# Optimization experiments

Measured on AMD Instinct MI355X. Metric: run time of the kernel, lower is better.

Reference implementation:

```python
import jax, jax.numpy as jnp
import numpy as np

DIM = 1024
N_HEADS = 16
B, S = 2, 2048


def setup_inputs() -> dict:
    key = jax.random.key(0)
    ks = jax.random.split(key, 9)
    scale = 1.0 / np.sqrt(DIM)
    return {
        "i1": jax.random.normal(ks[0], (B, S, DIM), jnp.float32),
        "i2": jax.random.normal(ks[1], (B, S, DIM), jnp.float32),
        "cr": jax.random.normal(ks[2], (B, S, 2), jnp.float32),
        # Linear params stored as [in, out] so forward is x @ W + b (same math as torch x W^T + b)
        "Wq": jax.random.normal(ks[3], (DIM, DIM), jnp.float32) * scale,
        "bq": jnp.zeros((DIM,), jnp.float32),
        "Wkv": jax.random.normal(ks[4], (DIM, 2 * DIM), jnp.float32) * scale,
        "bkv": jnp.zeros((2 * DIM,), jnp.float32),
        "Wmo": jax.random.normal(ks[5], (2, DIM), jnp.float32) * (1.0 / np.sqrt(2.0)),
        "bmo": jnp.zeros((DIM,), jnp.float32),
    }


def reference(i1, i2, cr, Wq, bq, Wkv, bkv, Wmo, bmo):
    H = N_HEADS
    Dh = DIM // H
    b, s, _ = i1.shape

    q = (i1 @ Wq + bq).reshape(b, s, H, Dh)                # [B,S,H,Dh]
    kv = i2 @ Wkv + bkv                                     # [B,S,2*DIM]
    k = kv[..., :DIM].reshape(b, s, H, Dh)
    v = kv[..., DIM:].reshape(b, s, H, Dh)
    mo = (cr @ Wmo + bmo).reshape(b, s, H, Dh)              # [B,S,H,Dh]

    scores = jnp.einsum("bqhd,bkhd->bhqk", q, k) / jnp.sqrt(jnp.asarray(Dh, q.dtype))
    probs = jax.nn.softmax(scores, axis=-1)                 # [B,H,S,S] (dropout p=0)

    h = jnp.einsum("bhqk,bkhd->bqhd", probs, v).reshape(b, s, DIM)
    m = jnp.einsum("bhqk,bkhd->bqhd", probs, mo).reshape(b, s, DIM)
    return h, m
```

## Files before the change

### kernel.cpp

```cpp
#include <hip/hip_runtime.h>
#include <hip/hip_bf16.h>

typedef __attribute__((ext_vector_type(8))) short short8;
typedef __attribute__((ext_vector_type(4))) short short4_t;
typedef __attribute__((ext_vector_type(4))) float f32x4;
typedef unsigned short ushort_t;

#define DEV __device__ __forceinline__

DEV ushort_t f2bf(float f) {
    unsigned u = __builtin_bit_cast(unsigned, f);
    u = u + 0x7fffu + ((u >> 16) & 1u);
    return (ushort_t)(u >> 16);
}

DEV unsigned pk_bf16(float lo, float hi) {
    __hip_bfloat162 h = __float22bfloat162_rn(make_float2(lo, hi));
    unsigned u;
    __builtin_memcpy(&u, &h, sizeof(u));
    return u;
}

DEV float fast_exp2(float x) {
#if __has_builtin(__builtin_amdgcn_exp2f)
    return __builtin_amdgcn_exp2f(x);
#else
    float r;
    asm("v_exp_f32 %0, %1" : "=v"(r) : "v"(x));
    return r;
#endif
}

DEV short8 ld8(const ushort_t* p) { return *reinterpret_cast<const short8*>(p); }

__global__ __launch_bounds__(256)
void cvt_bf16(const float* __restrict__ in, ushort_t* __restrict__ out)
{
    const size_t i = ((size_t)blockIdx.x * 256 + threadIdx.x) * 8;
    const float4 a = *reinterpret_cast<const float4*>(in + i);
    const float4 b = *reinterpret_cast<const float4*>(in + i + 4);
    short8 v;
    v[0] = (short)f2bf(a.x); v[1] = (short)f2bf(a.y);
    v[2] = (short)f2bf(a.z); v[3] = (short)f2bf(a.w);
    v[4] = (short)f2bf(b.x); v[5] = (short)f2bf(b.y);
    v[6] = (short)f2bf(b.z); v[7] = (short)f2bf(b.w);
    *reinterpret_cast<short8*>(out + i) = v;
}

__global__ __launch_bounds__(256)
void tcvt_bf16(const float* __restrict__ W, ushort_t* __restrict__ Wt, int K, int N)
{
    __shared__ ushort_t tile[64][72];
    const int t = threadIdx.x;
    const int nx = blockIdx.x * 64, ky = blockIdx.y * 64;
    const int r = t >> 2, q = (t & 3) * 16;

    const float* src = W + (size_t)(ky + r) * N + nx + q;
#pragma unroll
    for (int i = 0; i < 4; ++i) {
        const float4 v = *reinterpret_cast<const float4*>(src + 4 * i);
        tile[r][q + 4 * i + 0] = f2bf(v.x);
        tile[r][q + 4 * i + 1] = f2bf(v.y);
        tile[r][q + 4 * i + 2] = f2bf(v.z);
        tile[r][q + 4 * i + 3] = f2bf(v.w);
    }
    __syncthreads();
    short8 o0, o1;
#pragma unroll
    for (int i = 0; i < 8; ++i) {
        o0[i] = (short)tile[q + i][r];
        o1[i] = (short)tile[q + 8 + i][r];
    }
    ushort_t* dst = Wt + (size_t)(nx + r) * K + ky + q;
    *reinterpret_cast<short8*>(dst) = o0;
    *reinterpret_cast<short8*>(dst + 8) = o1;
}

__global__ __launch_bounds__(256, 2)
void proj_all(const ushort_t* __restrict__ A1, const ushort_t* __restrict__ A2,
              const ushort_t* __restrict__ Wqt, const ushort_t* __restrict__ Wkvt,
              const float* __restrict__ bqv, const float* __restrict__ bkv,
              ushort_t* __restrict__ Qr, ushort_t* __restrict__ Kr,
              ushort_t* __restrict__ Vt)
{
    __shared__ ushort_t As[128 * 72];
    __shared__ ushort_t Bs[128 * 72];

    const int t = threadIdx.x;
    const int lane = t & 63;
    const int wv = t >> 6;
    const int wr = wv >> 1, wc = wv & 1;
    const int c = lane & 15, g = lane >> 4;
    const int m0 = blockIdx.y * 128;
    const int nblk = blockIdx.x;

    const ushort_t* A;
    const ushort_t* Wt;
    const float* bias;
    int n0;
    if (nblk < 8) { A = A1; Wt = Wqt;  bias = bqv; n0 = nblk * 128; }
    else          { A = A2; Wt = Wkvt; bias = bkv; n0 = (nblk - 8) * 128; }
    const bool isQ = (nblk < 8);

    f32x4 acc[4][4];
    const f32x4 zero4 = {0.f, 0.f, 0.f, 0.f};
#pragma unroll
    for (int mi = 0; mi < 4; ++mi)
#pragma unroll
        for (int ni = 0; ni < 4; ++ni) acc[mi][ni] = zero4;

    const int srow[4] = { (t + 0)   >> 3, (t + 256) >> 3, (t + 512) >> 3, (t + 768) >> 3 };
    const int skq     = (t & 7) * 8;

    short8 a_reg[4], b_reg[4];
#pragma unroll
    for (int rep = 0; rep < 4; ++rep) {
        a_reg[rep] = ld8(A  + (size_t)(m0 + srow[rep]) * 1024 + skq);
        b_reg[rep] = ld8(Wt + (size_t)(n0 + srow[rep]) * 1024 + skq);
    }

    for (int it = 0; it < 16; ++it) {
#pragma unroll
        for (int rep = 0; rep < 4; ++rep) {
            *reinterpret_cast<short8*>(&As[srow[rep] * 72 + skq]) = a_reg[rep];
            *reinterpret_cast<short8*>(&Bs[srow[rep] * 72 + skq]) = b_reg[rep];
        }
        __syncthreads();
        if (it < 15) {
            const int k1 = (it + 1) * 64;
#pragma unroll
            for (int rep = 0; rep < 4; ++rep) {
                a_reg[rep] = ld8(A  + (size_t)(m0 + srow[rep]) * 1024 + k1 + skq);
                b_reg[rep] = ld8(Wt + (size_t)(n0 + srow[rep]) * 1024 + k1 + skq);
            }
        }
#pragma unroll
        for (int kk = 0; kk < 64; kk += 32) {
            short8 afr[4], bfr[4];
#pragma unroll
            for (int mi = 0; mi < 4; ++mi)
                afr[mi] = ld8(&As[(wr * 64 + mi * 16 + c) * 72 + kk + 8 * g]);
#pragma unroll
            for (int ni = 0; ni < 4; ++ni)
                bfr[ni] = ld8(&Bs[(wc * 64 + ni * 16 + c) * 72 + kk + 8 * g]);
#pragma unroll
            for (int mi = 0; mi < 4; ++mi)
#pragma unroll
                for (int ni = 0; ni < 4; ++ni)
                    acc[mi][ni] = __builtin_amdgcn_mfma_f32_16x16x32_bf16(
                        afr[mi], bfr[ni], acc[mi][ni], 0, 0, 0);
        }
        __syncthreads();
    }

#pragma unroll
    for (int mi = 0; mi < 4; ++mi) {
#pragma unroll
        for (int ni = 0; ni < 4; ++ni) {
            const int n = n0 + wc * 64 + ni * 16 + c;
            const float bb = bias[n];
#pragma unroll
            for (int j = 0; j < 4; ++j) {
                const int m = m0 + wr * 64 + mi * 16 + 4 * g + j;
                const int b = m >> 11, s = m & 2047;
                const ushort_t val = f2bf(acc[mi][ni][j] + bb);
                if (isQ) {
                    Qr[((size_t)((b * 16 + (n >> 6)) * 2048 + s)) * 64 + (n & 63)] = val;
                } else if (n < 1024) {
                    Kr[((size_t)((b * 16 + (n >> 6)) * 2048 + s)) * 64 + (n & 63)] = val;
                } else {
                    const int np = n - 1024;
                    Vt[(size_t)((b * 16 + (np >> 6)) * 64 + (np & 63)) * 2048 + s] = val;
                }
            }
        }
    }
}

__global__ __launch_bounds__(256)
void proj_gemm(const float* __restrict__ A, const float* __restrict__ W,
               const float* __restrict__ bias, int N,
               ushort_t* __restrict__ outRow, ushort_t* __restrict__ outT)
{
    __shared__ ushort_t As[128 * 72];
    __shared__ ushort_t Bt[128 * 72];

    const int t = threadIdx.x;
    const int lane = t & 63;
    const int wv = t >> 6;
    const int wr = wv >> 1, wc = wv & 1;
    const int c = lane & 15, g = lane >> 4;
    const int m0 = blockIdx.y * 128, n0 = blockIdx.x * 128;

    f32x4 acc[4][4];
    const f32x4 zero4 = {0.f, 0.f, 0.f, 0.f};
#pragma unroll
    for (int mi = 0; mi < 4; ++mi)
#pragma unroll
        for (int ni = 0; ni < 4; ++ni) acc[mi][ni] = zero4;

    for (int it = 0; it < 16; ++it) {
        const int k0 = it * 64;
        {
            const int kq = (t & 15) * 4;
            int r = t >> 4;
#pragma unroll
            for (int rep = 0; rep < 8; ++rep, r += 16) {
                float4 v = *reinterpret_cast<const float4*>(
                    A + (size_t)(m0 + r) * 1024 + k0 + kq);
                ushort_t* dst = &As[r * 72 + kq];
                dst[0] = f2bf(v.x); dst[1] = f2bf(v.y);
                dst[2] = f2bf(v.z); dst[3] = f2bf(v.w);
            }
        }
        {
            const int nq = (t & 31) * 4;
            const int kr = t >> 5;
#pragma unroll
            for (int rep = 0; rep < 8; ++rep) {
                const int k = kr + 8 * rep;
                float4 v = *reinterpret_cast<const float4*>(
                    W + (size_t)(k0 + k) * N + n0 + nq);
                Bt[(nq + 0) * 72 + k] = f2bf(v.x);
                Bt[(nq + 1) * 72 + k] = f2bf(v.y);
                Bt[(nq + 2) * 72 + k] = f2bf(v.z);
                Bt[(nq + 3) * 72 + k] = f2bf(v.w);
            }
        }
        __syncthreads();
#pragma unroll
        for (int kk = 0; kk < 64; kk += 32) {
            short8 afr[4], bfr[4];
#pragma unroll
            for (int mi = 0; mi < 4; ++mi)
                afr[mi] = ld8(&As[(wr * 64 + mi * 16 + c) * 72 + kk + 8 * g]);
#pragma unroll
            for (int ni = 0; ni < 4; ++ni)
                bfr[ni] = ld8(&Bt[(wc * 64 + ni * 16 + c) * 72 + kk + 8 * g]);
#pragma unroll
            for (int mi = 0; mi < 4; ++mi)
#pragma unroll
                for (int ni = 0; ni < 4; ++ni)
                    acc[mi][ni] = __builtin_amdgcn_mfma_f32_16x16x32_bf16(
                        afr[mi], bfr[ni], acc[mi][ni], 0, 0, 0);
        }
        __syncthreads();
    }

#pragma unroll
    for (int mi = 0; mi < 4; ++mi) {
#pragma unroll
        for (int ni = 0; ni < 4; ++ni) {
            const int n = n0 + wc * 64 + ni * 16 + c;
            const float bb = bias[n];
#pragma unroll
            for (int j = 0; j < 4; ++j) {
                const int m = m0 + wr * 64 + mi * 16 + 4 * g + j;
                const int b = m >> 11, s = m & 2047;
                const ushort_t val = f2bf(acc[mi][ni][j] + bb);
                if (outT != nullptr && n >= 1024) {
                    const int np = n - 1024;
                    const int hh = np >> 6, d = np & 63;
                    outT[(size_t)((b * 16 + hh) * 64 + d) * 2048 + s] = val;
                } else {
                    const int hh = n >> 6, d = n & 63;
                    outRow[((size_t)((b * 16 + hh) * 2048 + s)) * 64 + d] = val;
                }
            }
        }
    }
}

DEV void attn_body(const ushort_t* __restrict__ Kh, const ushort_t* __restrict__ Vh,
                   const float* __restrict__ crb, int kv_next,
                   const ushort_t* KsC, const ushort_t* VsC,
                   ushort_t* KsN, ushort_t* VsN,
                   int c, int g, int rk, int ck, int rv, int cv,
                   const short8 (&bq)[2][2],
                   float4 (&CC)[2][2], float4 (&CN)[2][2],
                   f32x4 (&accv)[2][4], float (&lst)[2],
                   float (&a0s)[2], float (&a1s)[2])
{
    const f32x4 zero4 = {0.f, 0.f, 0.f, 0.f};
    const float SCL = 0.18033688011112042f;

    const short8 kreg = ld8(Kh + (size_t)(kv_next + rk) * 64 + ck);
    const short8 vreg = ld8(Vh + (size_t)rv * 2048 + kv_next + cv);
    {
        const float* cp0 = crb + (size_t)(kv_next + 4 * g) * 2;
        CN[0][0] = *reinterpret_cast<const float4*>(cp0);
        CN[0][1] = *reinterpret_cast<const float4*>(cp0 + 4);
        const float* cp1 = crb + (size_t)(kv_next + 16 + 4 * g) * 2;
        CN[1][0] = *reinterpret_cast<const float4*>(cp1);
        CN[1][1] = *reinterpret_cast<const float4*>(cp1 + 4);
    }
    __builtin_amdgcn_sched_barrier(0);

    short8 KC[2][2];
#pragma unroll
    for (int ct = 0; ct < 2; ++ct)
#pragma unroll
        for (int st = 0; st < 2; ++st)
            KC[ct][st] = ld8(&KsC[(ct * 16 + c) * 72 + st * 32 + 8 * g]);
    short8 VC[4];
#pragma unroll
    for (int dt = 0; dt < 4; ++dt) {
        const short4_t vlo = *reinterpret_cast<const short4_t*>(&VsC[(dt * 16 + c) * 40 + 4 * g]);
        const short4_t vhi = *reinterpret_cast<const short4_t*>(&VsC[(dt * 16 + c) * 40 + 4 * g + 16]);
        VC[dt] = __builtin_shufflevector(vlo, vhi, 0, 1, 2, 3, 4, 5, 6, 7);
    }

    f32x4 sc[2][2];
#pragma unroll
    for (int qt = 0; qt < 2; ++qt)
#pragma unroll
        for (int ct = 0; ct < 2; ++ct) {
            f32x4 z = zero4;
            z = __builtin_amdgcn_mfma_f32_16x16x32_bf16(KC[ct][0], bq[qt][0], z, 0, 0, 0);
            z = __builtin_amdgcn_mfma_f32_16x16x32_bf16(KC[ct][1], bq[qt][1], z, 0, 0, 0);
            sc[qt][ct] = z;
        }

    short8 pa[2];
#pragma unroll
    for (int qt = 0; qt < 2; ++qt) {
        float e[2][4];
        float lc = lst[qt], a0c = a0s[qt], a1c = a1s[qt];
#pragma unroll
        for (int ct = 0; ct < 2; ++ct) {
            const float cr0[4] = {CC[ct][0].x, CC[ct][0].z, CC[ct][1].x, CC[ct][1].z};
            const float cr1[4] = {CC[ct][0].y, CC[ct][0].w, CC[ct][1].y, CC[ct][1].w};
#pragma unroll
            for (int j = 0; j < 4; ++j) {
                const float ev = fast_exp2(sc[qt][ct][j] * SCL);
                e[ct][j] = ev;
                lc  += ev;
                a0c += ev * cr0[j];
                a1c += ev * cr1[j];
            }
        }
        lst[qt] = lc; a0s[qt] = a0c; a1s[qt] = a1c;
        int4 w;
        w.x = (int)pk_bf16(e[0][0], e[0][1]);
        w.y = (int)pk_bf16(e[0][2], e[0][3]);
        w.z = (int)pk_bf16(e[1][0], e[1][1]);
        w.w = (int)pk_bf16(e[1][2], e[1][3]);
        pa[qt] = __builtin_bit_cast(short8, w);
    }

#pragma unroll
    for (int dt = 0; dt < 4; ++dt) {
        accv[0][dt] = __builtin_amdgcn_mfma_f32_16x16x32_bf16(VC[dt], pa[0], accv[0][dt], 0, 0, 0);
        accv[1][dt] = __builtin_amdgcn_mfma_f32_16x16x32_bf16(VC[dt], pa[1], accv[1][dt], 0, 0, 0);
    }

    *reinterpret_cast<short8*>(&KsN[rk * 72 + ck]) = kreg;
    *reinterpret_cast<short8*>(&VsN[rv * 40 + cv]) = vreg;
    __syncthreads();
}

__global__ __launch_bounds__(256, 2)
void attn_kernel(const ushort_t* __restrict__ Qr, const ushort_t* __restrict__ Kr,
                 const ushort_t* __restrict__ Vt, const float* __restrict__ cr,
                 const float* __restrict__ Wmo, const float* __restrict__ bmo,
                 float* __restrict__ out)
{
    __shared__ ushort_t Ks[2][32 * 72];
    __shared__ ushort_t Vs[2][64 * 40];

    const int t = threadIdx.x;
    const int w = t >> 6, lane = t & 63;
    const int c = lane & 15, g = lane >> 4;
    const int rk = t >> 3, ck = (t & 7) * 8;
    const int rv = t >> 2, cv = (t & 3) * 8;

    const int gid = blockIdx.x;
    const int bh = (gid & 7) + 8 * ((gid >> 3) & 3);
    const int xt = gid >> 5;
    const int b = bh >> 4, hh = bh & 15;
    const int qb = xt * 128 + w * 32;

    const ushort_t* Qh = Qr + (size_t)bh * (2048 * 64);
    const ushort_t* Kh = Kr + (size_t)bh * (2048 * 64);
    const ushort_t* Vh = Vt + (size_t)bh * (64 * 2048);
    const float*   crb = cr + (size_t)b * (2048 * 2);

    short8 bq[2][2];
#pragma unroll
    for (int qt = 0; qt < 2; ++qt)
#pragma unroll
        for (int st = 0; st < 2; ++st)
            bq[qt][st] = ld8(Qh + (size_t)(qb + qt * 16 + c) * 64 + st * 32 + 8 * g);

    f32x4 accv[2][4];
    const f32x4 zero4 = {0.f, 0.f, 0.f, 0.f};
#pragma unroll
    for (int qt = 0; qt < 2; ++qt)
#pragma unroll
        for (int dt = 0; dt < 4; ++dt) accv[qt][dt] = zero4;

    float lst[2] = {0.f, 0.f};
    float a0s[2] = {0.f, 0.f};
    float a1s[2] = {0.f, 0.f};

    float4 cA[2][2], cB[2][2];

    {
        const short8 k0 = ld8(Kh + (size_t)rk * 64 + ck);
        const short8 v0 = ld8(Vh + (size_t)rv * 2048 + cv);
        *reinterpret_cast<short8*>(&Ks[0][rk * 72 + ck]) = k0;
        *reinterpret_cast<short8*>(&Vs[0][rv * 40 + cv]) = v0;
        const float* cp0 = crb + (size_t)(4 * g) * 2;
        cA[0][0] = *reinterpret_cast<const float4*>(cp0);
        cA[0][1] = *reinterpret_cast<const float4*>(cp0 + 4);
        const float* cp1 = crb + (size_t)(16 + 4 * g) * 2;
        cA[1][0] = *reinterpret_cast<const float4*>(cp1);
        cA[1][1] = *reinterpret_cast<const float4*>(cp1 + 4);
    }
    __syncthreads();

    for (int i = 0; i < 32; ++i) {
        const int kvb = i * 64;
        attn_body(Kh, Vh, crb, kvb + 32,
                  &Ks[0][0], &Vs[0][0], &Ks[1][0], &Vs[1][0],
                  c, g, rk, ck, rv, cv, bq, cA, cB,
                  accv, lst, a0s, a1s);
        attn_body(Kh, Vh, crb, (kvb + 64) & 2047,
                  &Ks[1][0], &Vs[1][0], &Ks[0][0], &Vs[0][0],
                  c, g, rk, ck, rv, cv, bq, cB, cA,
                  accv, lst, a0s, a1s);
    }

#pragma unroll
    for (int qt = 0; qt < 2; ++qt) {
        lst[qt] += __shfl_xor(lst[qt], 16, 64); lst[qt] += __shfl_xor(lst[qt], 32, 64);
        a0s[qt] += __shfl_xor(a0s[qt], 16, 64); a0s[qt] += __shfl_xor(a0s[qt], 32, 64);
        a1s[qt] += __shfl_xor(a1s[qt], 16, 64); a1s[qt] += __shfl_xor(a1s[qt], 32, 64);
    }

#pragma unroll
    for (int qt = 0; qt < 2; ++qt) {
        const int q = qb + qt * 16 + c;
        const float inv = 1.f / lst[qt];
        const float a0 = a0s[qt] * inv, a1 = a1s[qt] * inv;
#pragma unroll
        for (int dt = 0; dt < 4; ++dt) {
            const int d = hh * 64 + dt * 16 + 4 * g;
            const float4 w0 = *reinterpret_cast<const float4*>(Wmo + d);
            const float4 w1 = *reinterpret_cast<const float4*>(Wmo + 1024 + d);
            const float4 bm = *reinterpret_cast<const float4*>(bmo + d);
            const size_t oidx = ((size_t)(b * 2048 + q)) * 1024 + d;
            float4 hv, mv;
            hv.x = accv[qt][dt][0] * inv; hv.y = accv[qt][dt][1] * inv;
            hv.z = accv[qt][dt][2] * inv; hv.w = accv[qt][dt][3] * inv;
            mv.x = a0 * w0.x + a1 * w1.x + bm.x;
            mv.y = a0 * w0.y + a1 * w1.y + bm.y;
            mv.z = a0 * w0.z + a1 * w1.z + bm.z;
            mv.w = a0 * w0.w + a1 * w1.w + bm.w;
            *reinterpret_cast<float4*>(out + oidx) = hv;
            *reinterpret_cast<float4*>(out + 4194304 + oidx) = mv;
        }
    }
}

extern "C" void kernel_launch(void* const* d_in, const int* in_sizes, int n_in,
                              void* d_out, int out_size, void* d_ws, size_t ws_size,
                              hipStream_t stream)
{
    const float* i1  = (const float*)d_in[0];
    const float* i2  = (const float*)d_in[1];
    const float* cr  = (const float*)d_in[2];
    const float* Wq  = (const float*)d_in[3];
    const float* bq  = (const float*)d_in[4];
    const float* Wkv = (const float*)d_in[5];
    const float* bkv = (const float*)d_in[6];
    const float* Wmo = (const float*)d_in[7];
    const float* bmo = (const float*)d_in[8];
    float* out = (float*)d_out;

    ushort_t* Qr = (ushort_t*)d_ws;
    ushort_t* Kr = Qr + 4194304;
    ushort_t* Vt = Kr + 4194304;

    if (ws_size >= 48234496ULL) {
        ushort_t* A1   = Vt + 4194304;
        ushort_t* A2   = A1 + 4194304;
        ushort_t* Wqt  = A2 + 4194304;
        ushort_t* Wkvt = Wqt + 1048576;
        cvt_bf16<<<dim3(2048), dim3(256), 0, stream>>>(i1, A1);
        cvt_bf16<<<dim3(2048), dim3(256), 0, stream>>>(i2, A2);
        tcvt_bf16<<<dim3(16, 16), dim3(256), 0, stream>>>(Wq, Wqt, 1024, 1024);
        tcvt_bf16<<<dim3(32, 16), dim3(256), 0, stream>>>(Wkv, Wkvt, 1024, 2048);
        proj_all<<<dim3(24, 32), dim3(256), 0, stream>>>(A1, A2, Wqt, Wkvt, bq, bkv, Qr, Kr, Vt);
    } else {
        proj_gemm<<<dim3(8, 32), dim3(256), 0, stream>>>(i1, Wq, bq, 1024, Qr, nullptr);
        proj_gemm<<<dim3(16, 32), dim3(256), 0, stream>>>(i2, Wkv, bkv, 2048, Kr, Vt);
    }
    attn_kernel<<<dim3(512), dim3(256), 0, stream>>>(Qr, Kr, Vt, cr, Wmo, bmo, out);
}
```

Before: 132.4 us.

## Split attention KV range across warp pairs and double grid size

Each block now handles 64 queries instead of 128, and its four warps split into two query groups times two KV halves. Each warp pair streams half of the 2048 keys into its own double-buffered shared tiles. Partial accumulators, row sums and cr-weighted sums are then merged through shared memory before the epilogue. The grid doubles to 1024 blocks and launch bounds ask for 4 blocks per CU, raising parallelism and occupancy. In exchange, each K/V tile is loaded by twice as many blocks, there is an extra reduction step, and the tighter occupancy target adds register pressure.

```diff
diff --git a/kernel.cpp b/kernel.cpp
--- a/kernel.cpp
+++ b/kernel.cpp
@@ -271,11 +271,13 @@
     }
 }
 
-DEV void attn_body(const ushort_t* __restrict__ Kh, const ushort_t* __restrict__ Vh,
-                   const float* __restrict__ crb, int kv_next,
+DEV void attn_body(const ushort_t* __restrict__ khh, const ushort_t* __restrict__ vhh,
+                   const float* __restrict__ crh, int kv_next,
                    const ushort_t* KsC, const ushort_t* VsC,
                    ushort_t* KsN, ushort_t* VsN,
-                   int c, int g, int rk, int ck, int rv, int cv,
+                   int c, int g,
+                   int krow0, int krow1, int kcol,
+                   int vrow0, int vrow1, int vcol,
                    const short8 (&bq)[2][2],
                    float4 (&CC)[2][2], float4 (&CN)[2][2],
                    f32x4 (&accv)[2][4], float (&lst)[2],
@@ -284,13 +286,15 @@
     const f32x4 zero4 = {0.f, 0.f, 0.f, 0.f};
     const float SCL = 0.18033688011112042f;
 
-    const short8 kreg = ld8(Kh + (size_t)(kv_next + rk) * 64 + ck);
-    const short8 vreg = ld8(Vh + (size_t)rv * 2048 + kv_next + cv);
+    const short8 kreg0 = ld8(khh + (size_t)(kv_next + krow0) * 64 + kcol);
+    const short8 kreg1 = ld8(khh + (size_t)(kv_next + krow1) * 64 + kcol);
+    const short8 vreg0 = ld8(vhh + (size_t)vrow0 * 2048 + kv_next + vcol);
+    const short8 vreg1 = ld8(vhh + (size_t)vrow1 * 2048 + kv_next + vcol);
     {
-        const float* cp0 = crb + (size_t)(kv_next + 4 * g) * 2;
+        const float* cp0 = crh + (size_t)(kv_next + 4 * g) * 2;
         CN[0][0] = *reinterpret_cast<const float4*>(cp0);
         CN[0][1] = *reinterpret_cast<const float4*>(cp0 + 4);
-        const float* cp1 = crb + (size_t)(kv_next + 16 + 4 * g) * 2;
+        const float* cp1 = crh + (size_t)(kv_next + 16 + 4 * g) * 2;
         CN[1][0] = *reinterpret_cast<const float4*>(cp1);
         CN[1][1] = *reinterpret_cast<const float4*>(cp1 + 4);
     }
@@ -354,37 +358,51 @@
         accv[1][dt] = __builtin_amdgcn_mfma_f32_16x16x32_bf16(VC[dt], pa[1], accv[1][dt], 0, 0, 0);
     }
 
-    *reinterpret_cast<short8*>(&KsN[rk * 72 + ck]) = kreg;
-    *reinterpret_cast<short8*>(&VsN[rv * 40 + cv]) = vreg;
+    *reinterpret_cast<short8*>(&KsN[krow0 * 72 + kcol]) = kreg0;
+    *reinterpret_cast<short8*>(&KsN[krow1 * 72 + kcol]) = kreg1;
+    *reinterpret_cast<short8*>(&VsN[vrow0 * 40 + vcol]) = vreg0;
+    *reinterpret_cast<short8*>(&VsN[vrow1 * 40 + vcol]) = vreg1;
     __syncthreads();
 }
 
-__global__ __launch_bounds__(256, 2)
+__global__ __launch_bounds__(256, 4)
 void attn_kernel(const ushort_t* __restrict__ Qr, const ushort_t* __restrict__ Kr,
                  const ushort_t* __restrict__ Vt, const float* __restrict__ cr,
                  const float* __restrict__ Wmo, const float* __restrict__ bmo,
                  float* __restrict__ out)
 {
-    __shared__ ushort_t Ks[2][32 * 72];
-    __shared__ ushort_t Vs[2][64 * 40];
+    __shared__ short8 smem16[2432];
+    ushort_t* smem = (ushort_t*)smem16;
 
     const int t = threadIdx.x;
     const int w = t >> 6, lane = t & 63;
+    const int wq = w & 1, wk = w >> 1;
     const int c = lane & 15, g = lane >> 4;
-    const int rk = t >> 3, ck = (t & 7) * 8;
-    const int rv = t >> 2, cv = (t & 3) * 8;
+    const int th = t & 127;
+
+    const int krow0 = th >> 3,          krow1 = (th + 128) >> 3, kcol = (th & 7) * 8;
+    const int vrow0 = th >> 2,          vrow1 = (th + 128) >> 2, vcol = (th & 3) * 8;
 
     const int gid = blockIdx.x;
     const int bh = (gid & 7) + 8 * ((gid >> 3) & 3);
     const int xt = gid >> 5;
     const int b = bh >> 4, hh = bh & 15;
-    const int qb = xt * 128 + w * 32;
+    const int qb = xt * 64 + wq * 32;
 
     const ushort_t* Qh = Qr + (size_t)bh * (2048 * 64);
     const ushort_t* Kh = Kr + (size_t)bh * (2048 * 64);
     const ushort_t* Vh = Vt + (size_t)bh * (64 * 2048);
     const float*   crb = cr + (size_t)b * (2048 * 2);
 
+    const ushort_t* khh = Kh + (size_t)(wk * 1024) * 64;
+    const ushort_t* vhh = Vh + wk * 1024;
+    const float*    crh = crb + (size_t)(wk * 1024) * 2;
+
+    ushort_t* Kbuf0 = smem + (wk * 2 + 0) * 2304;
+    ushort_t* Kbuf1 = smem + (wk * 2 + 1) * 2304;
+    ushort_t* Vbuf0 = smem + 9216 + (wk * 2 + 0) * 2560;
+    ushort_t* Vbuf1 = smem + 9216 + (wk * 2 + 1) * 2560;
+
     short8 bq[2][2];
 #pragma unroll
     for (int qt = 0; qt < 2; ++qt)
@@ -406,33 +424,58 @@
     float4 cA[2][2], cB[2][2];
 
     {
-        const short8 k0 = ld8(Kh + (size_t)rk * 64 + ck);
-        const short8 v0 = ld8(Vh + (size_t)rv * 2048 + cv);
-        *reinterpret_cast<short8*>(&Ks[0][rk * 72 + ck]) = k0;
-        *reinterpret_cast<short8*>(&Vs[0][rv * 40 + cv]) = v0;
-        const float* cp0 = crb + (size_t)(4 * g) * 2;
+        *reinterpret_cast<short8*>(&Kbuf0[krow0 * 72 + kcol]) =
+            ld8(khh + (size_t)krow0 * 64 + kcol);
+        *reinterpret_cast<short8*>(&Kbuf0[krow1 * 72 + kcol]) =
+            ld8(khh + (size_t)krow1 * 64 + kcol);
+        *reinterpret_cast<short8*>(&Vbuf0[vrow0 * 40 + vcol]) =
+            ld8(vhh + (size_t)vrow0 * 2048 + vcol);
+        *reinterpret_cast<short8*>(&Vbuf0[vrow1 * 40 + vcol]) =
+            ld8(vhh + (size_t)vrow1 * 2048 + vcol);
+        const float* cp0 = crh + (size_t)(4 * g) * 2;
         cA[0][0] = *reinterpret_cast<const float4*>(cp0);
         cA[0][1] = *reinterpret_cast<const float4*>(cp0 + 4);
-        const float* cp1 = crb + (size_t)(16 + 4 * g) * 2;
+        const float* cp1 = crh + (size_t)(16 + 4 * g) * 2;
         cA[1][0] = *reinterpret_cast<const float4*>(cp1);
         cA[1][1] = *reinterpret_cast<const float4*>(cp1 + 4);
     }
     __syncthreads();
 
-    for (int i = 0; i < 32; ++i) {
+    for (int i = 0; i < 16; ++i) {
         const int kvb = i * 64;
-        attn_body(Kh, Vh, crb, kvb + 32,
-                  &Ks[0][0], &Vs[0][0], &Ks[1][0], &Vs[1][0],
-                  c, g, rk, ck, rv, cv, bq, cA, cB,
-                  accv, lst, a0s, a1s);
-        attn_body(Kh, Vh, crb, (kvb + 64) & 2047,
-                  &Ks[1][0], &Vs[1][0], &Ks[0][0], &Vs[0][0],
-                  c, g, rk, ck, rv, cv, bq, cB, cA,
-                  accv, lst, a0s, a1s);
-    }
+        attn_body(khh, vhh, crh, kvb + 32,
+                  Kbuf0, Vbuf0, Kbuf1, Vbuf1,
+                  c, g, krow0, krow1, kcol, vrow0, vrow1, vcol,
+                  bq, cA, cB, accv, lst, a0s, a1s);
+        attn_body(khh, vhh, crh, (kvb + 64) & 1023,
+                  Kbuf1, Vbuf1, Kbuf0, Vbuf0,
+                  c, g, krow0, krow1, kcol, vrow0, vrow1, vcol,
+                  bq, cB, cA, accv, lst, a0s, a1s);
+    }
+
+    float* my = reinterpret_cast<float*>(smem16) + ((size_t)(wq * 64 + lane)) * 40;
+    if (wk == 1) {
+#pragma unroll
+        for (int qt = 0; qt < 2; ++qt)
+#pragma unroll
+            for (int dt = 0; dt < 4; ++dt)
+#pragma unroll
+                for (int j = 0; j < 4; ++j) my[qt * 16 + dt * 4 + j] = accv[qt][dt][j];
+#pragma unroll
+        for (int qt = 0; qt < 2; ++qt) {
+            my[32 + qt] = lst[qt]; my[34 + qt] = a0s[qt]; my[36 + qt] = a1s[qt];
+        }
+    }
+    __syncthreads();
+    if (wk != 0) return;
 
 #pragma unroll
     for (int qt = 0; qt < 2; ++qt) {
+#pragma unroll
+        for (int dt = 0; dt < 4; ++dt)
+#pragma unroll
+            for (int j = 0; j < 4; ++j) accv[qt][dt][j] += my[qt * 16 + dt * 4 + j];
+        lst[qt] += my[32 + qt]; a0s[qt] += my[34 + qt]; a1s[qt] += my[36 + qt];
         lst[qt] += __shfl_xor(lst[qt], 16, 64); lst[qt] += __shfl_xor(lst[qt], 32, 64);
         a0s[qt] += __shfl_xor(a0s[qt], 16, 64); a0s[qt] += __shfl_xor(a0s[qt], 32, 64);
         a1s[qt] += __shfl_xor(a1s[qt], 16, 64); a1s[qt] += __shfl_xor(a1s[qt], 32, 64);
@@ -496,5 +539,5 @@
         proj_gemm<<<dim3(8, 32), dim3(256), 0, stream>>>(i1, Wq, bq, 1024, Qr, nullptr);
         proj_gemm<<<dim3(16, 32), dim3(256), 0, stream>>>(i2, Wkv, bkv, 2048, Kr, Vt);
     }
-    attn_kernel<<<dim3(512), dim3(256), 0, stream>>>(Qr, Kr, Vt, cr, Wmo, bmo, out);
-}
+    attn_kernel<<<dim3(1024), dim3(256), 0, stream>>>(Qr, Kr, Vt, cr, Wmo, bmo, out);
+}
```

Result: slower. 397.4 us, median of 2 (+200.3%).

## Split attention KV range in two and merge partials in a second kernel

Applied to the files above, without the earlier changes.

Adds an attention kernel in which each block handles half of the key/value sequence, doubling the grid from 512 to 1024 blocks so more of the GPU's compute units are busy. Partial unnormalized outputs and row statistics go to workspace, and a merge kernel sums the two halves, normalizes, and computes the mo projection output. This adds a kernel launch and about 32 MB of extra global traffic for the partials. It is only used when the workspace is large enough, otherwise the original kernel runs.

```diff
diff --git a/kernel.cpp b/kernel.cpp
--- a/kernel.cpp
+++ b/kernel.cpp
@@ -423,12 +423,10 @@
         const int kvb = i * 64;
         attn_body(Kh, Vh, crb, kvb + 32,
                   &Ks[0][0], &Vs[0][0], &Ks[1][0], &Vs[1][0],
-                  c, g, rk, ck, rv, cv, bq, cA, cB,
-                  accv, lst, a0s, a1s);
+                  c, g, rk, ck, rv, cv, bq, cA, cB, accv, lst, a0s, a1s);
         attn_body(Kh, Vh, crb, (kvb + 64) & 2047,
                   &Ks[1][0], &Vs[1][0], &Ks[0][0], &Vs[0][0],
-                  c, g, rk, ck, rv, cv, bq, cB, cA,
-                  accv, lst, a0s, a1s);
+                  c, g, rk, ck, rv, cv, bq, cB, cA, accv, lst, a0s, a1s);
     }
 
 #pragma unroll
@@ -463,6 +461,139 @@
     }
 }
 
+__global__ __launch_bounds__(256, 2)
+void attn_split(const ushort_t* __restrict__ Qr, const ushort_t* __restrict__ Kr,
+                const ushort_t* __restrict__ Vt, const float* __restrict__ cr,
+                float* __restrict__ ph, float4* __restrict__ pst)
+{
+    __shared__ ushort_t Ks[2][32 * 72];
+    __shared__ ushort_t Vs[2][64 * 40];
+
+    const int t = threadIdx.x;
+    const int w = t >> 6, lane = t & 63;
+    const int c = lane & 15, g = lane >> 4;
+    const int rk = t >> 3, ck = (t & 7) * 8;
+    const int rv = t >> 2, cv = (t & 3) * 8;
+
+    const int gid = blockIdx.x;
+    const int bh = (gid & 7) + 8 * ((gid >> 3) & 3);
+    const int rest = gid >> 5;
+    const int half = rest & 1;
+    const int xt = rest >> 1;
+    const int qb = xt * 128 + w * 32;
+
+    const ushort_t* Qh = Qr + (size_t)bh * (2048 * 64);
+    const ushort_t* Kh = Kr + (size_t)bh * (2048 * 64) + (size_t)(half * 1024) * 64;
+    const ushort_t* Vh = Vt + (size_t)bh * (64 * 2048) + half * 1024;
+    const float*   crb = cr + (size_t)(bh >> 4) * (2048 * 2) + (size_t)(half * 1024) * 2;
+
+    short8 bq[2][2];
+#pragma unroll
+    for (int qt = 0; qt < 2; ++qt)
+#pragma unroll
+        for (int st = 0; st < 2; ++st)
+            bq[qt][st] = ld8(Qh + (size_t)(qb + qt * 16 + c) * 64 + st * 32 + 8 * g);
+
+    f32x4 accv[2][4];
+    const f32x4 zero4 = {0.f, 0.f, 0.f, 0.f};
+#pragma unroll
+    for (int qt = 0; qt < 2; ++qt)
+#pragma unroll
+        for (int dt = 0; dt < 4; ++dt) accv[qt][dt] = zero4;
+
+    float lst[2] = {0.f, 0.f};
+    float a0s[2] = {0.f, 0.f};
+    float a1s[2] = {0.f, 0.f};
+
+    float4 cA[2][2], cB[2][2];
+
+    {
+        const short8 k0 = ld8(Kh + (size_t)rk * 64 + ck);
+        const short8 v0 = ld8(Vh + (size_t)rv * 2048 + cv);
+        *reinterpret_cast<short8*>(&Ks[0][rk * 72 + ck]) = k0;
+        *reinterpret_cast<short8*>(&Vs[0][rv * 40 + cv]) = v0;
+        const float* cp0 = crb + (size_t)(4 * g) * 2;
+        cA[0][0] = *reinterpret_cast<const float4*>(cp0);
+        cA[0][1] = *reinterpret_cast<const float4*>(cp0 + 4);
+        const float* cp1 = crb + (size_t)(16 + 4 * g) * 2;
+        cA[1][0] = *reinterpret_cast<const float4*>(cp1);
+        cA[1][1] = *reinterpret_cast<const float4*>(cp1 + 4);
+    }
+    __syncthreads();
+
+    for (int i = 0; i < 16; ++i) {
+        const int kvb = i * 64;
+        attn_body(Kh, Vh, crb, kvb + 32,
+                  &Ks[0][0], &Vs[0][0], &Ks[1][0], &Vs[1][0],
+                  c, g, rk, ck, rv, cv, bq, cA, cB, accv, lst, a0s, a1s);
+        attn_body(Kh, Vh, crb, (kvb + 64) & 1023,
+                  &Ks[1][0], &Vs[1][0], &Ks[0][0], &Vs[0][0],
+                  c, g, rk, ck, rv, cv, bq, cB, cA, accv, lst, a0s, a1s);
+    }
+
+#pragma unroll
+    for (int qt = 0; qt < 2; ++qt) {
+        lst[qt] += __shfl_xor(lst[qt], 16, 64); lst[qt] += __shfl_xor(lst[qt], 32, 64);
+        a0s[qt] += __shfl_xor(a0s[qt], 16, 64); a0s[qt] += __shfl_xor(a0s[qt], 32, 64);
+        a1s[qt] += __shfl_xor(a1s[qt], 16, 64); a1s[qt] += __shfl_xor(a1s[qt], 32, 64);
+    }
+
+    const size_t hbase = ((size_t)half * 32 + bh) * 2048;
+#pragma unroll
+    for (int qt = 0; qt < 2; ++qt) {
+        const int q = qb + qt * 16 + c;
+        float* pq = ph + (hbase + q) * 64;
+#pragma unroll
+        for (int dt = 0; dt < 4; ++dt) {
+            float4 hv;
+            hv.x = accv[qt][dt][0]; hv.y = accv[qt][dt][1];
+            hv.z = accv[qt][dt][2]; hv.w = accv[qt][dt][3];
+            *reinterpret_cast<float4*>(pq + dt * 16 + 4 * g) = hv;
+        }
+        if (g == 0)
+            pst[hbase + q] = make_float4(lst[qt], a0s[qt], a1s[qt], 0.f);
+    }
+}
+
+__global__ __launch_bounds__(256)
+void merge_kernel(const float* __restrict__ ph, const float4* __restrict__ pst,
+                  const float* __restrict__ Wmo, const float* __restrict__ bmo,
+                  float* __restrict__ out)
+{
+    const size_t tid = (size_t)blockIdx.x * 256 + threadIdx.x;
+    const int d4 = (int)(tid & 15);
+    const int q  = (int)((tid >> 4) & 2047);
+    const int bh = (int)(tid >> 15);
+    const int b = bh >> 4, hh = bh & 15;
+
+    const size_t base = (size_t)bh * 2048 + q;
+    const float4 h0 = *reinterpret_cast<const float4*>(ph + base * 64 + d4 * 4);
+    const float4 h1 = *reinterpret_cast<const float4*>(ph + (base + 65536) * 64 + d4 * 4);
+    const float4 s0 = pst[base];
+    const float4 s1 = pst[base + 65536];
+
+    const float inv = 1.f / (s0.x + s1.x);
+    const float a0 = (s0.y + s1.y) * inv;
+    const float a1 = (s0.z + s1.z) * inv;
+
+    const int d = hh * 64 + d4 * 4;
+    const float4 w0 = *reinterpret_cast<const float4*>(Wmo + d);
+    const float4 w1 = *reinterpret_cast<const float4*>(Wmo + 1024 + d);
+    const float4 bm = *reinterpret_cast<const float4*>(bmo + d);
+
+    float4 hv, mv;
+    hv.x = (h0.x + h1.x) * inv; hv.y = (h0.y + h1.y) * inv;
+    hv.z = (h0.z + h1.z) * inv; hv.w = (h0.w + h1.w) * inv;
+    mv.x = a0 * w0.x + a1 * w1.x + bm.x;
+    mv.y = a0 * w0.y + a1 * w1.y + bm.y;
+    mv.z = a0 * w0.z + a1 * w1.z + bm.z;
+    mv.w = a0 * w0.w + a1 * w1.w + bm.w;
+
+    const size_t oidx = ((size_t)(b * 2048 + q)) * 1024 + d;
+    *reinterpret_cast<float4*>(out + oidx) = hv;
+    *reinterpret_cast<float4*>(out + 4194304 + oidx) = mv;
+}
+
 extern "C" void kernel_launch(void* const* d_in, const int* in_sizes, int n_in,
                               void* d_out, int out_size, void* d_ws, size_t ws_size,
                               hipStream_t stream)
@@ -481,12 +612,17 @@
     ushort_t* Qr = (ushort_t*)d_ws;
     ushort_t* Kr = Qr + 4194304;
     ushort_t* Vt = Kr + 4194304;
-
-    if (ws_size >= 48234496ULL) {
-        ushort_t* A1   = Vt + 4194304;
-        ushort_t* A2   = A1 + 4194304;
-        ushort_t* Wqt  = A2 + 4194304;
-        ushort_t* Wkvt = Wqt + 1048576;
+    ushort_t* A1   = Vt + 4194304;
+    ushort_t* A2   = A1 + 4194304;
+    ushort_t* Wqt  = A2 + 4194304;
+    ushort_t* Wkvt = Wqt + 1048576;
+    float*  ph  = (float*)(Vt + 4194304);
+    float4* pst = (float4*)(ph + 8388608);
+
+    const size_t WS_FAST  = 48234496ULL;
+    const size_t WS_SPLIT = 60817408ULL;
+
+    if (ws_size >= WS_FAST) {
         cvt_bf16<<<dim3(2048), dim3(256), 0, stream>>>(i1, A1);
         cvt_bf16<<<dim3(2048), dim3(256), 0, stream>>>(i2, A2);
         tcvt_bf16<<<dim3(16, 16), dim3(256), 0, stream>>>(Wq, Wqt, 1024, 1024);
@@ -496,5 +632,11 @@
         proj_gemm<<<dim3(8, 32), dim3(256), 0, stream>>>(i1, Wq, bq, 1024, Qr, nullptr);
         proj_gemm<<<dim3(16, 32), dim3(256), 0, stream>>>(i2, Wkv, bkv, 2048, Kr, Vt);
     }
-    attn_kernel<<<dim3(512), dim3(256), 0, stream>>>(Qr, Kr, Vt, cr, Wmo, bmo, out);
-}
+
+    if (ws_size >= WS_SPLIT) {
+        attn_split<<<dim3(1024), dim3(256), 0, stream>>>(Qr, Kr, Vt, cr, ph, pst);
+        merge_kernel<<<dim3(4096), dim3(256), 0, stream>>>(ph, pst, Wmo, bmo, out);
+    } else {
+        attn_kernel<<<dim3(512), dim3(256), 0, stream>>>(Qr, Kr, Vt, cr, Wmo, bmo, out);
+    }
+}
```

After: 141.9 us. 1.07x slower.

## Process two KV tiles per barrier with quad-buffered LDS and staged cr values

Applied to the files above, without the earlier changes.

The attention loop now handles two 32-key tiles per synchronization step. It uses four LDS buffers for K, V and the cr coordinates, prefetching the next pair from global memory while computing the current pair. The cr values are now staged through shared memory by the first wave instead of each thread loading them from global memory. This halves the number of __syncthreads and lengthens the window that hides load latency. In exchange it uses more LDS and registers, which could reduce occupancy at two blocks per CU.

```diff
diff --git a/kernel.cpp b/kernel.cpp
--- a/kernel.cpp
+++ b/kernel.cpp
@@ -271,43 +271,34 @@
     }
 }
 
-DEV void attn_body(const ushort_t* __restrict__ Kh, const ushort_t* __restrict__ Vh,
-                   const float* __restrict__ crb, int kv_next,
-                   const ushort_t* KsC, const ushort_t* VsC,
-                   ushort_t* KsN, ushort_t* VsN,
-                   int c, int g, int rk, int ck, int rv, int cv,
-                   const short8 (&bq)[2][2],
-                   float4 (&CC)[2][2], float4 (&CN)[2][2],
-                   f32x4 (&accv)[2][4], float (&lst)[2],
-                   float (&a0s)[2], float (&a1s)[2])
+DEV void tile_compute(const ushort_t* __restrict__ Ks, const ushort_t* __restrict__ Vs,
+                      const float* __restrict__ Crs, int c, int g,
+                      const short8 (&bq)[2][2],
+                      f32x4 (&accv)[2][4], float (&lst)[2],
+                      float (&a0s)[2], float (&a1s)[2])
 {
     const f32x4 zero4 = {0.f, 0.f, 0.f, 0.f};
     const float SCL = 0.18033688011112042f;
 
-    const short8 kreg = ld8(Kh + (size_t)(kv_next + rk) * 64 + ck);
-    const short8 vreg = ld8(Vh + (size_t)rv * 2048 + kv_next + cv);
-    {
-        const float* cp0 = crb + (size_t)(kv_next + 4 * g) * 2;
-        CN[0][0] = *reinterpret_cast<const float4*>(cp0);
-        CN[0][1] = *reinterpret_cast<const float4*>(cp0 + 4);
-        const float* cp1 = crb + (size_t)(kv_next + 16 + 4 * g) * 2;
-        CN[1][0] = *reinterpret_cast<const float4*>(cp1);
-        CN[1][1] = *reinterpret_cast<const float4*>(cp1 + 4);
-    }
-    __builtin_amdgcn_sched_barrier(0);
-
     short8 KC[2][2];
 #pragma unroll
     for (int ct = 0; ct < 2; ++ct)
 #pragma unroll
         for (int st = 0; st < 2; ++st)
-            KC[ct][st] = ld8(&KsC[(ct * 16 + c) * 72 + st * 32 + 8 * g]);
+            KC[ct][st] = ld8(&Ks[(ct * 16 + c) * 72 + st * 32 + 8 * g]);
     short8 VC[4];
 #pragma unroll
     for (int dt = 0; dt < 4; ++dt) {
-        const short4_t vlo = *reinterpret_cast<const short4_t*>(&VsC[(dt * 16 + c) * 40 + 4 * g]);
-        const short4_t vhi = *reinterpret_cast<const short4_t*>(&VsC[(dt * 16 + c) * 40 + 4 * g + 16]);
+        const short4_t vlo = *reinterpret_cast<const short4_t*>(&Vs[(dt * 16 + c) * 40 + 4 * g]);
+        const short4_t vhi = *reinterpret_cast<const short4_t*>(&Vs[(dt * 16 + c) * 40 + 4 * g + 16]);
         VC[dt] = __builtin_shufflevector(vlo, vhi, 0, 1, 2, 3, 4, 5, 6, 7);
+    }
+    float4 cc[2][2];
+#pragma unroll
+    for (int ct = 0; ct < 2; ++ct) {
+        const float4* cp = reinterpret_cast<const float4*>(Crs + (16 * ct + 4 * g) * 2);
+        cc[ct][0] = cp[0];
+        cc[ct][1] = cp[1];
     }
 
     f32x4 sc[2][2];
@@ -328,8 +319,8 @@
         float lc = lst[qt], a0c = a0s[qt], a1c = a1s[qt];
 #pragma unroll
         for (int ct = 0; ct < 2; ++ct) {
-            const float cr0[4] = {CC[ct][0].x, CC[ct][0].z, CC[ct][1].x, CC[ct][1].z};
-            const float cr1[4] = {CC[ct][0].y, CC[ct][0].w, CC[ct][1].y, CC[ct][1].w};
+            const float cr0[4] = {cc[ct][0].x, cc[ct][0].z, cc[ct][1].x, cc[ct][1].z};
+            const float cr1[4] = {cc[ct][0].y, cc[ct][0].w, cc[ct][1].y, cc[ct][1].w};
 #pragma unroll
             for (int j = 0; j < 4; ++j) {
                 const float ev = fast_exp2(sc[qt][ct][j] * SCL);
@@ -353,9 +344,41 @@
         accv[0][dt] = __builtin_amdgcn_mfma_f32_16x16x32_bf16(VC[dt], pa[0], accv[0][dt], 0, 0, 0);
         accv[1][dt] = __builtin_amdgcn_mfma_f32_16x16x32_bf16(VC[dt], pa[1], accv[1][dt], 0, 0, 0);
     }
-
-    *reinterpret_cast<short8*>(&KsN[rk * 72 + ck]) = kreg;
-    *reinterpret_cast<short8*>(&VsN[rv * 40 + cv]) = vreg;
+}
+
+DEV void pair_body(const ushort_t* __restrict__ Kh, const ushort_t* __restrict__ Vh,
+                   const float* __restrict__ crb, int kvA, int kvB,
+                   const ushort_t* KsC0, const ushort_t* VsC0, const float* CrC0,
+                   const ushort_t* KsC1, const ushort_t* VsC1, const float* CrC1,
+                   ushort_t* KsN0, ushort_t* VsN0, float* CrN0,
+                   ushort_t* KsN1, ushort_t* VsN1, float* CrN1,
+                   int t, int c, int g, int rk, int ck, int rv, int cv,
+                   const short8 (&bq)[2][2],
+                   f32x4 (&accv)[2][4], float (&lst)[2],
+                   float (&a0s)[2], float (&a1s)[2])
+{
+    const short8 kregA = ld8(Kh + (size_t)(kvA + rk) * 64 + ck);
+    const short8 vregA = ld8(Vh + (size_t)rv * 2048 + kvA + cv);
+    const short8 kregB = ld8(Kh + (size_t)(kvB + rk) * 64 + ck);
+    const short8 vregB = ld8(Vh + (size_t)rv * 2048 + kvB + cv);
+    float2 crreg = make_float2(0.f, 0.f);
+    if (t < 64) {
+        const int kvX = (t & 32) ? kvB : kvA;
+        crreg = *reinterpret_cast<const float2*>(crb + (size_t)(kvX + (t & 31)) * 2);
+    }
+    __builtin_amdgcn_sched_barrier(0);
+
+    tile_compute(KsC0, VsC0, CrC0, c, g, bq, accv, lst, a0s, a1s);
+    tile_compute(KsC1, VsC1, CrC1, c, g, bq, accv, lst, a0s, a1s);
+
+    *reinterpret_cast<short8*>(&KsN0[rk * 72 + ck]) = kregA;
+    *reinterpret_cast<short8*>(&VsN0[rv * 40 + cv]) = vregA;
+    *reinterpret_cast<short8*>(&KsN1[rk * 72 + ck]) = kregB;
+    *reinterpret_cast<short8*>(&VsN1[rv * 40 + cv]) = vregB;
+    if (t < 64) {
+        float* d = (t & 32) ? CrN1 : CrN0;
+        *reinterpret_cast<float2*>(d + (t & 31) * 2) = crreg;
+    }
     __syncthreads();
 }
 
@@ -365,8 +388,13 @@
                  const float* __restrict__ Wmo, const float* __restrict__ bmo,
                  float* __restrict__ out)
 {
-    __shared__ ushort_t Ks[2][32 * 72];
-    __shared__ ushort_t Vs[2][64 * 40];
+    __shared__ ushort_t smem[19968];
+    ushort_t* K0 = smem;            ushort_t* K1 = smem + 2304;
+    ushort_t* K2 = smem + 4608;     ushort_t* K3 = smem + 6912;
+    ushort_t* V0 = smem + 9216;     ushort_t* V1 = smem + 11776;
+    ushort_t* V2 = smem + 14336;    ushort_t* V3 = smem + 16896;
+    float* C0 = reinterpret_cast<float*>(smem + 19456);
+    float* C1 = C0 + 64;  float* C2 = C0 + 128;  float* C3 = C0 + 192;
 
     const int t = threadIdx.x;
     const int w = t >> 6, lane = t & 63;
@@ -403,32 +431,30 @@
     float a0s[2] = {0.f, 0.f};
     float a1s[2] = {0.f, 0.f};
 
-    float4 cA[2][2], cB[2][2];
-
     {
-        const short8 k0 = ld8(Kh + (size_t)rk * 64 + ck);
-        const short8 v0 = ld8(Vh + (size_t)rv * 2048 + cv);
-        *reinterpret_cast<short8*>(&Ks[0][rk * 72 + ck]) = k0;
-        *reinterpret_cast<short8*>(&Vs[0][rv * 40 + cv]) = v0;
-        const float* cp0 = crb + (size_t)(4 * g) * 2;
-        cA[0][0] = *reinterpret_cast<const float4*>(cp0);
-        cA[0][1] = *reinterpret_cast<const float4*>(cp0 + 4);
-        const float* cp1 = crb + (size_t)(16 + 4 * g) * 2;
-        cA[1][0] = *reinterpret_cast<const float4*>(cp1);
-        cA[1][1] = *reinterpret_cast<const float4*>(cp1 + 4);
+        *reinterpret_cast<short8*>(&K0[rk * 72 + ck]) = ld8(Kh + (size_t)rk * 64 + ck);
+        *reinterpret_cast<short8*>(&V0[rv * 40 + cv]) = ld8(Vh + (size_t)rv * 2048 + cv);
+        *reinterpret_cast<short8*>(&K1[rk * 72 + ck]) = ld8(Kh + (size_t)(32 + rk) * 64 + ck);
+        *reinterpret_cast<short8*>(&V1[rv * 40 + cv]) = ld8(Vh + (size_t)rv * 2048 + 32 + cv);
+        if (t < 64) {
+            const int kvX = (t & 32) ? 32 : 0;
+            const float2 v = *reinterpret_cast<const float2*>(crb + (size_t)(kvX + (t & 31)) * 2);
+            float* d = (t & 32) ? C1 : C0;
+            *reinterpret_cast<float2*>(d + (t & 31) * 2) = v;
+        }
     }
     __syncthreads();
 
-    for (int i = 0; i < 32; ++i) {
-        const int kvb = i * 64;
-        attn_body(Kh, Vh, crb, kvb + 32,
-                  &Ks[0][0], &Vs[0][0], &Ks[1][0], &Vs[1][0],
-                  c, g, rk, ck, rv, cv, bq, cA, cB,
-                  accv, lst, a0s, a1s);
-        attn_body(Kh, Vh, crb, (kvb + 64) & 2047,
-                  &Ks[1][0], &Vs[1][0], &Ks[0][0], &Vs[0][0],
-                  c, g, rk, ck, rv, cv, bq, cB, cA,
-                  accv, lst, a0s, a1s);
+    for (int i = 0; i < 16; ++i) {
+        const int base = i * 128;
+        pair_body(Kh, Vh, crb, base + 64, base + 96,
+                  K0, V0, C0, K1, V1, C1,
+                  K2, V2, C2, K3, V3, C3,
+                  t, c, g, rk, ck, rv, cv, bq, accv, lst, a0s, a1s);
+        pair_body(Kh, Vh, crb, (base + 128) & 2047, (base + 160) & 2047,
+                  K2, V2, C2, K3, V3, C3,
+                  K0, V0, C0, K1, V1, C1,
+                  t, c, g, rk, ck, rv, cv, bq, accv, lst, a0s, a1s);
     }
 
 #pragma unroll
```

Result: faster. 122.2 us (-7.7%).
